# Kernel tuning notes

Hardware: AMD Instinct MI355X
Metric: run time of the kernel (lower is better)

Reference implementation:

```python
import jax, jax.numpy as jnp
import numpy as np

NUM_SAMPLES = 5      # samples per line (line_matcher_cfg)
MIN_DIST_PTS = 8.0   # min pixel spacing between samples
TOP_K = 10           # top-k candidate lines for NW matching
GRID_SIZE = 4        # desc map stride
GAP = 0.1            # NW gap penalty


def sample_line_points(line_seg):
    # line_seg: (N, 2, 2) ij endpoints -> pts (N, S, 2), valid (N, S)
    start, end = line_seg[:, 0], line_seg[:, 1]
    lengths = jnp.linalg.norm(end - start, axis=1)
    nsamp = jnp.clip(jnp.floor(lengths / MIN_DIST_PTS), 2.0, float(NUM_SAMPLES))
    k = jnp.arange(NUM_SAMPLES, dtype=line_seg.dtype)
    interval = (end - start) / (nsamp - 1.0)[:, None]          # (N, 2)
    pts = start[:, None, :] + k[None, :, None] * interval[:, None, :]
    valid = k[None, :] < nsamp[:, None]
    pts = jnp.where(valid[..., None], pts, 0.0)                # torch pads with 0
    return pts, valid


def sample_descriptors(desc, pts):
    # Faithful F.grid_sample(bilinear, zeros padding, align_corners=False) after
    # kornia normalize_pixel_coordinates ((size-1) normalization), then L2-norm.
    # desc: (1, D, H, W); pts: (P, 2) ij coords in full-res image.
    D, H, W = desc.shape[1], desc.shape[2], desc.shape[3]
    img_h, img_w = H * GRID_SIZE, W * GRID_SIZE
    xn = 2.0 * pts[:, 1] / (img_w - 1) - 1.0
    yn = 2.0 * pts[:, 0] / (img_h - 1) - 1.0
    ix = ((xn + 1.0) * W - 1.0) / 2.0   # align_corners=False unnormalize
    iy = ((yn + 1.0) * H - 1.0) / 2.0
    x0f = jnp.floor(ix); y0f = jnp.floor(iy)
    wx = ix - x0f; wy = iy - y0f
    x0 = x0f.astype(jnp.int32); y0 = y0f.astype(jnp.int32)
    img = desc[0]

    def gather(xi, yi):
        inb = ((xi >= 0) & (xi < W) & (yi >= 0) & (yi < H)).astype(img.dtype)
        xc = jnp.clip(xi, 0, W - 1); yc = jnp.clip(yi, 0, H - 1)
        return img[:, yc, xc] * inb[None, :]   # (D, P), zeros outside

    v = (gather(x0, y0) * ((1 - wx) * (1 - wy))[None]
         + gather(x0 + 1, y0) * (wx * (1 - wy))[None]
         + gather(x0, y0 + 1) * ((1 - wx) * wy)[None]
         + gather(x0 + 1, y0 + 1) * (wx * wy)[None])
    return v / jnp.linalg.norm(v, axis=0, keepdims=True)


def needleman_wunsch(scores):
    # scores: (B, n, m); sequential DP via nested lax.scan (rows, then cols)
    B, n, m = scores.shape
    s = jnp.transpose(scores, (1, 0, 2)) - GAP  # (n, B, m)

    def row_step(prev_row, srow):               # prev_row (B, m+1), srow (B, m)
        diag = prev_row[:, :-1].T                # (m, B)
        up = prev_row[:, 1:].T                   # (m, B)

        def col_step(left, xs):
            d, u, sc = xs
            cur = jnp.maximum(jnp.maximum(left, u), d + sc)
            return cur, cur

        _, cols = jax.lax.scan(col_step, jnp.zeros((B,), s.dtype), (diag, up, srow.T))
        new_row = jnp.concatenate([jnp.zeros((B, 1), s.dtype), cols.T], axis=1)
        return new_row, None

    final, _ = jax.lax.scan(row_step, jnp.zeros((B, m + 1), s.dtype), s)
    return final[:, -1]


def filter_and_match_lines(scores):
    # scores: (N, M, n, n)
    ls1 = scores.max(3); v1 = (ls1 != -1.0).astype(scores.dtype)
    ls1 = (ls1 * v1).sum(2) / v1.sum(2)
    ls2 = scores.max(2); v2 = (ls2 != -1.0).astype(scores.dtype)
    ls2 = (ls2 * v2).sum(2) / v2.sum(2)
    line_scores = (ls1 + ls2) / 2.0
    topk_lines = jnp.argsort(line_scores, axis=1)[:, -TOP_K:]          # (N, k)
    top = jnp.take_along_axis(scores, topk_lines[:, :, None, None], axis=1)
    top = jnp.concatenate([top, jnp.flip(top, axis=-1)], axis=1)       # (N, 2k, n, n)
    N, top2k, n, m = top.shape
    nw = needleman_wunsch(top.reshape(N * top2k, n, m)).reshape(N, top2k)
    matches = jnp.argmax(nw, axis=1) % (top2k // 2)
    matches = topk_lines[jnp.arange(N), matches]
    return matches, nw


def match_forward(line_seg1, line_seg2, desc1, desc2):
    N, M = line_seg1.shape[0], line_seg2.shape[0]
    pts1, val1 = sample_line_points(line_seg1)
    pts2, val2 = sample_line_points(line_seg2)
    d1 = sample_descriptors(desc1, pts1.reshape(-1, 2))   # (D, N*S)
    d2 = sample_descriptors(desc2, pts2.reshape(-1, 2))   # (D, M*S)
    scores = d1.T @ d2                                    # (N*S, M*S)
    scores = jnp.where(val1.reshape(-1)[:, None], scores, -1.0)
    scores = jnp.where(val2.reshape(-1)[None, :], scores, -1.0)
    scores = scores.reshape(N, NUM_SAMPLES, M, NUM_SAMPLES).transpose(0, 2, 1, 3)
    matches, nw = filter_and_match_lines(scores)
    # cross check
    matches2, _ = filter_and_match_lines(scores.transpose(1, 0, 3, 2))
    mutual = matches2[matches] == jnp.arange(N)
    matches = jnp.where(mutual, matches, -1)
    return matches, nw


def setup_inputs():
    key = jax.random.key(0)
    k1, k2, k3, k4 = jax.random.split(key, 4)
    N = M = 1200; D = 128; H = W = 128
    img = float(H * GRID_SIZE - 1)
    line_seg1 = jax.random.uniform(k1, (N, 2, 2), jnp.float32) * img
    line_seg2 = jax.random.uniform(k2, (M, 2, 2), jnp.float32) * img
    desc1 = jax.random.normal(k3, (1, D, H, W), jnp.float32)
    desc2 = jax.random.normal(k4, (1, D, H, W), jnp.float32)
    return {"line_seg1": line_seg1, "line_seg2": line_seg2, "desc1": desc1, "desc2": desc2}


def reference(line_seg1, line_seg2, desc1, desc2):
    return match_forward(line_seg1, line_seg2, desc1, desc2)
```

## Files before the change

kernel.cpp:

```cpp
#include <hip/hip_runtime.h>
#include <hip/hip_bf16.h>


#define NLINES 1200
#define NS 5
#define DD 128
#define HH 128
#define WW 128
#define HW (HH*WW)
#define IMGM1 511.0f
#define GAPC 0.1f
#define NPAD 1216
#define PPAD (NPAD*NS)
#define KEXT 384
#define NCH (KEXT/32)
#define NGRP (PPAD/16)

typedef __attribute__((ext_vector_type(8))) short short8;
typedef __attribute__((ext_vector_type(4))) float f32x4;

__global__ void transpose_desc(const float* __restrict__ in1, float* __restrict__ out1,
                               const float* __restrict__ in2, float* __restrict__ out2) {
    const float* in = blockIdx.z ? in2 : in1;
    float* out = blockIdx.z ? out2 : out1;
    __shared__ float t[32][33];
    int s0 = blockIdx.x * 32;
    int d0 = blockIdx.y * 32;
    int c = threadIdx.x;
    int r0 = threadIdx.y;
    #pragma unroll
    for (int rr = 0; rr < 32; rr += 8) {
        int d = d0 + r0 + rr;
        t[r0 + rr][c] = in[d * HW + s0 + c];
    }
    __syncthreads();
    #pragma unroll
    for (int rr = 0; rr < 32; rr += 8) {
        int s = s0 + r0 + rr;
        out[s * DD + d0 + c] = t[c][r0 + rr];
    }
}

__global__ void samplepack_kernel(const float* __restrict__ lseg1, const float* __restrict__ lseg2,
                                  const float* __restrict__ tdesc1, const float* __restrict__ tdesc2,
                                  const float* __restrict__ desc1, const float* __restrict__ desc2,
                                  short* __restrict__ Aext, short* __restrict__ Bext,
                                  float* __restrict__ val1, float* __restrict__ val2,
                                  int use_t) {
    int side = blockIdx.y;
    const float* lseg = side ? lseg2 : lseg1;
    const float* tdesc = side ? tdesc2 : tdesc1;
    const float* desc = side ? desc2 : desc1;
    short* Ef = side ? Bext : Aext;
    float* valout = side ? val2 : val1;
    int arole = side ? 0 : 1;

    __shared__ float ds[16][129];
    int g = blockIdx.x;
    int t = threadIdx.x;
    int lane = t & 63, w = t >> 6;

    #pragma unroll
    for (int s = 0; s < 4; ++s) {
        int r = w * 4 + s;
        int pt = g * 16 + r;
        int line = pt / NS;
        int k = pt - line * NS;

        float sy = 0.f, sx = 0.f, ey = 0.f, ex = 0.f;
        if (line < NLINES) {
            sy = lseg[line * 4 + 0]; sx = lseg[line * 4 + 1];
            ey = lseg[line * 4 + 2]; ex = lseg[line * 4 + 3];
        }
        float dy = ey - sy, dx = ex - sx;
        float len = sqrtf(dy * dy + dx * dx);
        float ns = floorf(len * 0.125f);
        ns = fminf(fmaxf(ns, 2.0f), 5.0f);
        float kf = (float)k;
        float validf = (kf < ns) ? 1.0f : 0.0f;
        float py = sy + kf * (dy / (ns - 1.0f));
        float px = sx + kf * (dx / (ns - 1.0f));
        if (validf == 0.0f) { py = 0.0f; px = 0.0f; }

        float xn = 2.0f * px / IMGM1 - 1.0f;
        float yn = 2.0f * py / IMGM1 - 1.0f;
        float ix = ((xn + 1.0f) * (float)WW - 1.0f) * 0.5f;
        float iy = ((yn + 1.0f) * (float)HH - 1.0f) * 0.5f;
        float x0f = floorf(ix), y0f = floorf(iy);
        float wx = ix - x0f, wy = iy - y0f;
        int x0 = (int)x0f, y0 = (int)y0f;

        float w00 = (1.0f - wx) * (1.0f - wy);
        float w10 = wx * (1.0f - wy);
        float w01 = (1.0f - wx) * wy;
        float w11 = wx * wy;

        float v0 = 0.0f, v1 = 0.0f;
        int xs[4] = { x0, x0 + 1, x0,     x0 + 1 };
        int ys[4] = { y0, y0,     y0 + 1, y0 + 1 };
        float ws4[4] = { w00, w10, w01, w11 };
        #pragma unroll
        for (int c = 0; c < 4; ++c) {
            int xi = xs[c], yi = ys[c];
            float inb = (xi >= 0 && xi < WW && yi >= 0 && yi < HH) ? 1.0f : 0.0f;
            int xc = min(max(xi, 0), WW - 1);
            int yc = min(max(yi, 0), HH - 1);
            if (use_t) {
                int base = (yc * WW + xc) * DD;
                v0 += tdesc[base + lane] * inb * ws4[c];
                v1 += tdesc[base + 64 + lane] * inb * ws4[c];
            } else {
                int base = yc * WW + xc;
                v0 += desc[lane * HW + base] * inb * ws4[c];
                v1 += desc[(lane + 64) * HW + base] * inb * ws4[c];
            }
        }
        float ss = v0 * v0 + v1 * v1;
        #pragma unroll
        for (int o = 32; o > 0; o >>= 1) ss += __shfl_xor(ss, o);
        if (ss == 0.0f) ss = 1.0f;
        float nrm = sqrtf(ss);
        ds[r][lane] = v0 / nrm;
        ds[r][64 + lane] = v1 / nrm;
        if (lane == 0) valout[pt] = (line < NLINES) ? validf : 0.0f;
    }
    __syncthreads();

    #pragma unroll
    for (int it = 0; it < 3; ++it) {
        int idx = it * 256 + t;
        int c = idx >> 6, l = idx & 63;
        int q = l >> 4, r = l & 15;
        short8 outv;
        #pragma unroll
        for (int jj = 0; jj < 8; ++jj) {
            int kext = c * 32 + q * 8 + jj;
            int term = kext >> 7, k = kext & 127;
            float x = ds[r][k];
            __hip_bfloat16 h = __float2bfloat16(x);
            short v = *(short*)&h;
            bool lo_term = arole ? (term == 1) : (term == 2);
            if (lo_term) {
                float hf = __bfloat162float(h);
                __hip_bfloat16 lw = __float2bfloat16(x - hf);
                v = *(short*)&lw;
            }
            outv[jj] = v;
        }
        *(short8*)&Ef[((size_t)(g * NCH + c) * 64 + l) * 8] = outv;
    }
}

__launch_bounds__(256, 2)
__global__ void score_kernel(const short* __restrict__ Af, const short* __restrict__ Bf,
                             const float* __restrict__ val1, const float* __restrict__ val2,
                             float* __restrict__ lsc, float* __restrict__ lscT) {
    __shared__ float dump[80 * 161];

    const int t = threadIdx.x;
    const int lane = t & 63;
    const int w = t >> 6;
    const int wm = w >> 1;
    const int wn = w & 1;
    const int gA0 = blockIdx.x * 10;
    const int gB0 = blockIdx.y * 10;

    const short* pa[5];
    const short* pb[5];
    #pragma unroll
    for (int ti = 0; ti < 5; ++ti) {
        pa[ti] = Af + ((size_t)(gA0 + 5 * wm + ti) * NCH * 64 + lane) * 8;
        pb[ti] = Bf + ((size_t)(gB0 + 5 * wn + ti) * NCH * 64 + lane) * 8;
    }

    f32x4 acc[5][5];
    #pragma unroll
    for (int a = 0; a < 5; ++a)
        #pragma unroll
        for (int b = 0; b < 5; ++b)
            acc[a][b] = (f32x4){0.f, 0.f, 0.f, 0.f};

    short8 ca[5], cb[5], na[5], nb[5];
    #pragma unroll
    for (int ti = 0; ti < 5; ++ti) {
        ca[ti] = *(const short8*)(pa[ti]);
        cb[ti] = *(const short8*)(pb[ti]);
    }
    #pragma unroll
    for (int c = 0; c < NCH; c += 2) {
        #pragma unroll
        for (int ti = 0; ti < 5; ++ti) {
            na[ti] = *(const short8*)(pa[ti] + (c + 1) * 512);
            nb[ti] = *(const short8*)(pb[ti] + (c + 1) * 512);
        }
        #pragma unroll
        for (int ti = 0; ti < 5; ++ti)
            #pragma unroll
            for (int tj = 0; tj < 5; ++tj)
                acc[ti][tj] = __builtin_amdgcn_mfma_f32_16x16x32_bf16(
                    ca[ti], cb[tj], acc[ti][tj], 0, 0, 0);
        if (c + 2 < NCH) {
            #pragma unroll
            for (int ti = 0; ti < 5; ++ti) {
                ca[ti] = *(const short8*)(pa[ti] + (c + 2) * 512);
                cb[ti] = *(const short8*)(pb[ti] + (c + 2) * 512);
            }
        }
        #pragma unroll
        for (int ti = 0; ti < 5; ++ti)
            #pragma unroll
            for (int tj = 0; tj < 5; ++tj)
                acc[ti][tj] = __builtin_amdgcn_mfma_f32_16x16x32_bf16(
                    na[ti], nb[tj], acc[ti][tj], 0, 0, 0);
    }

    const int i0l = blockIdx.x * 32;
    const int j0l = blockIdx.y * 32;
    #pragma unroll
    for (int p = 0; p < 2; ++p) {
        __syncthreads();
        if (wm == p) {
            #pragma unroll
            for (int ti = 0; ti < 5; ++ti) {
                #pragma unroll
                for (int reg = 0; reg < 4; ++reg) {
                    int rloc = 16 * ti + (lane >> 4) * 4 + reg;
                    #pragma unroll
                    for (int tj = 0; tj < 5; ++tj) {
                        int col = 80 * wn + 16 * tj + (lane & 15);
                        dump[rloc * 161 + col] = acc[ti][tj][reg];
                    }
                }
            }
        }
        __syncthreads();
        #pragma unroll
        for (int e = 0; e < 2; ++e) {
            int q = t * 2 + e;
            int li = q >> 5, lj = q & 31;
            int i = i0l + 16 * p + li;
            int j = j0l + lj;
            if (i < NLINES && j < NLINES) {
                float S[5][5];
                #pragma unroll
                for (int a = 0; a < 5; ++a) {
                    float va = val1[i * NS + a];
                    #pragma unroll
                    for (int b = 0; b < 5; ++b) {
                        float vb = val2[j * NS + b];
                        float sc = dump[(li * 5 + a) * 161 + (lj * 5 + b)];
                        S[a][b] = (va != 0.0f && vb != 0.0f) ? sc : -1.0f;
                    }
                }
                float sum1 = 0.0f, cnt1 = 0.0f;
                #pragma unroll
                for (int a = 0; a < 5; ++a) {
                    float r = S[a][0];
                    #pragma unroll
                    for (int b = 1; b < 5; ++b) r = fmaxf(r, S[a][b]);
                    float v = (r != -1.0f) ? 1.0f : 0.0f;
                    sum1 += r * v; cnt1 += v;
                }
                float sum2 = 0.0f, cnt2 = 0.0f;
                #pragma unroll
                for (int b = 0; b < 5; ++b) {
                    float r = S[0][b];
                    #pragma unroll
                    for (int a = 1; a < 5; ++a) r = fmaxf(r, S[a][b]);
                    float v = (r != -1.0f) ? 1.0f : 0.0f;
                    sum2 += r * v; cnt2 += v;
                }
                lsc[i * NLINES + j] = (sum1 / cnt1 + sum2 / cnt2) * 0.5f;
            }
        }
        #pragma unroll
        for (int e = 0; e < 2; ++e) {
            int q = t * 2 + e;
            int lj = q >> 4, li = q & 15;
            int i = i0l + 16 * p + li;
            int j = j0l + lj;
            if (i < NLINES && j < NLINES) {
                float S[5][5];
                #pragma unroll
                for (int a = 0; a < 5; ++a) {
                    float va = val1[i * NS + a];
                    #pragma unroll
                    for (int b = 0; b < 5; ++b) {
                        float vb = val2[j * NS + b];
                        float sc = dump[(li * 5 + a) * 161 + (lj * 5 + b)];
                        S[a][b] = (va != 0.0f && vb != 0.0f) ? sc : -1.0f;
                    }
                }
                float sum1 = 0.0f, cnt1 = 0.0f;
                #pragma unroll
                for (int a = 0; a < 5; ++a) {
                    float r = S[a][0];
                    #pragma unroll
                    for (int b = 1; b < 5; ++b) r = fmaxf(r, S[a][b]);
                    float v = (r != -1.0f) ? 1.0f : 0.0f;
                    sum1 += r * v; cnt1 += v;
                }
                float sum2 = 0.0f, cnt2 = 0.0f;
                #pragma unroll
                for (int b = 0; b < 5; ++b) {
                    float r = S[0][b];
                    #pragma unroll
                    for (int a = 1; a < 5; ++a) r = fmaxf(r, S[a][b]);
                    float v = (r != -1.0f) ? 1.0f : 0.0f;
                    sum2 += r * v; cnt2 += v;
                }
                lscT[j * NLINES + i] = (sum1 / cnt1 + sum2 / cnt2) * 0.5f;
            }
        }
    }
}

__global__ void topk_kernel(const float* __restrict__ lsc, const float* __restrict__ lscT,
                            int* __restrict__ topk1, int* __restrict__ topk2) {
    __shared__ float wv[4];
    __shared__ int wi[4];
    int rb = blockIdx.x;
    const float* ls = (rb < NLINES) ? (lsc + rb * NLINES) : (lscT + (rb - NLINES) * NLINES);
    int* topk = (rb < NLINES) ? (topk1 + rb * 10) : (topk2 + (rb - NLINES) * 10);
    int t = threadIdx.x;
    int lane = t & 63, w = t >> 6;
    float val[5];
    #pragma unroll
    for (int s = 0; s < 5; ++s) {
        int j = t + 256 * s;
        val[s] = (j < NLINES) ? ls[j] : -1e30f;
    }
    float bv = -1e30f; int bi = -1;
    #pragma unroll
    for (int s = 0; s < 5; ++s) {
        int j = t + 256 * s;
        if (val[s] >= bv) { bv = val[s]; bi = j; }
    }
    for (int sel = 0; sel < 10; ++sel) {
        float rv = bv; int ri = bi;
        #pragma unroll
        for (int o = 32; o > 0; o >>= 1) {
            float ov = __shfl_xor(rv, o);
            int oi = __shfl_xor(ri, o);
            if (ov > rv || (ov == rv && oi > ri)) { rv = ov; ri = oi; }
        }
        if (lane == 0) { wv[w] = rv; wi[w] = ri; }
        __syncthreads();
        float fv = wv[0]; int fi = wi[0];
        #pragma unroll
        for (int qq = 1; qq < 4; ++qq)
            if (wv[qq] > fv || (wv[qq] == fv && wi[qq] > fi)) { fv = wv[qq]; fi = wi[qq]; }
        if (t == 0) topk[9 - sel] = fi;
        if ((fi & 255) == t) {
            val[fi >> 8] = -1e30f;
            bv = -1e30f; bi = -1;
            #pragma unroll
            for (int s = 0; s < 5; ++s) {
                int j = t + 256 * s;
                if (val[s] >= bv) { bv = val[s]; bi = j; }
            }
        }
        __syncthreads();
    }
}

__device__ __forceinline__ float nw5(const float* M) {
    float F[6] = {0, 0, 0, 0, 0, 0};
    #pragma unroll
    for (int x = 0; x < 5; ++x) {
        float diag = F[0];
        float left = 0.0f;
        #pragma unroll
        for (int y = 1; y <= 5; ++y) {
            float up = F[y];
            float cur = fmaxf(fmaxf(left, up), diag + (M[x * 5 + y - 1] - GAPC));
            F[y] = cur; left = cur; diag = up;
        }
    }
    return F[5];
}

__global__ void nw_kernel(const short* __restrict__ Af, const short* __restrict__ Bf,
                          const float* __restrict__ val1, const float* __restrict__ val2,
                          const int* __restrict__ topk1, const int* __restrict__ topk2,
                          float* __restrict__ nwout, float* __restrict__ nw2buf) {
    __shared__ float sbuf[10][25];
    __shared__ int jl[10];
    int rb = blockIdx.x;
    int dir = (rb >= NLINES) ? 1 : 0;
    int row = rb - dir * NLINES;
    int lane = threadIdx.x;
    int q = lane >> 4, rr = lane & 15;

    if (lane < 10) jl[lane] = (dir ? topk2 : topk1)[row * 10 + lane];
    __syncthreads();

    const short* shEf = dir ? Bf : Af;
    const short* cdEf = dir ? Af : Bf;

    int ptS = row * 5 + min(rr, 4);
    const short* shp = shEf + ((size_t)(ptS >> 4) * NCH * 64 + q * 16 + (ptS & 15)) * 8;
    short8 sh[NCH];
    #pragma unroll
    for (int c = 0; c < NCH; ++c) sh[c] = *(const short8*)(shp + c * 512);

    #pragma unroll
    for (int pp = 0; pp < 5; ++pp) {
        int c1 = jl[2 * pp], c2 = jl[2 * pp + 1];
        int ptC = (rr < 8) ? (c1 * 5 + min(rr, 4)) : (c2 * 5 + min(rr - 8, 4));
        const short* cp = cdEf + ((size_t)(ptC >> 4) * NCH * 64 + q * 16 + (ptC & 15)) * 8;
        f32x4 acc = (f32x4){0.f, 0.f, 0.f, 0.f};
        #pragma unroll
        for (int c = 0; c < NCH; ++c) {
            short8 cb = *(const short8*)(cp + c * 512);
            acc = dir ? __builtin_amdgcn_mfma_f32_16x16x32_bf16(cb, sh[c], acc, 0, 0, 0)
                      : __builtin_amdgcn_mfma_f32_16x16x32_bf16(sh[c], cb, acc, 0, 0, 0);
        }
        #pragma unroll
        for (int reg = 0; reg < 4; ++reg) {
            int m = q * 4 + reg, n = rr;
            if (!dir) {
                if (m < 5 && n < 5) sbuf[2 * pp][m * 5 + n] = acc[reg];
                if (m < 5 && n >= 8 && n < 13) sbuf[2 * pp + 1][m * 5 + (n - 8)] = acc[reg];
            } else {
                if (m < 5 && n < 5) sbuf[2 * pp][m * 5 + n] = acc[reg];
                if (m >= 8 && m < 13 && n < 5) sbuf[2 * pp + 1][(m - 8) * 5 + n] = acc[reg];
            }
        }
    }
    __syncthreads();

    if (lane < 20) {
        int r = lane >> 1, rev = lane & 1;
        int i = dir ? jl[r] : row;
        int j = dir ? row : jl[r];
        float S[25];
        #pragma unroll
        for (int a = 0; a < 5; ++a) {
            float va = val1[i * NS + a];
            #pragma unroll
            for (int b = 0; b < 5; ++b) {
                float vb = val2[j * NS + b];
                S[a * 5 + b] = (va != 0.0f && vb != 0.0f) ? sbuf[r][a * 5 + b] : -1.0f;
            }
        }
        float M[25];
        #pragma unroll
        for (int x = 0; x < 5; ++x)
            #pragma unroll
            for (int y = 0; y < 5; ++y) {
                if (!dir) M[x * 5 + y] = rev ? S[x * 5 + (4 - y)] : S[x * 5 + y];
                else      M[x * 5 + y] = rev ? S[(4 - y) * 5 + x] : S[y * 5 + x];
            }
        float nwv = nw5(M);
        float* o = dir ? nw2buf : nwout;
        o[row * 20 + rev * 10 + r] = nwv;
    }
}

__global__ void argmax_final_kernel(const float* __restrict__ nw1, const float* __restrict__ nw2,
                                    const int* __restrict__ topk1, const int* __restrict__ topk2,
                                    float* __restrict__ out) {
    __shared__ int mpre[NLINES];
    __shared__ int m2[NLINES];
    int t = threadIdx.x;
    for (int qq = t; qq < 2 * NLINES; qq += 1024) {
        int dir = qq / NLINES, row = qq - dir * NLINES;
        const float* nw = (dir ? nw2 : nw1) + row * 20;
        float best = nw[0]; int bi = 0;
        #pragma unroll
        for (int q = 1; q < 20; ++q) {
            float v = nw[q];
            if (v > best) { best = v; bi = q; }
        }
        int m = (dir ? topk2 : topk1)[row * 10 + (bi % 10)];
        if (dir) m2[row] = m; else mpre[row] = m;
    }
    __syncthreads();
    for (int i = t; i < NLINES; i += 1024) {
        int m = mpre[i];
        out[i] = (m2[m] == i) ? (float)m : -1.0f;
    }
}

extern "C" void kernel_launch(void* const* d_in, const int* in_sizes, int n_in,
                              void* d_out, int out_size, void* d_ws, size_t ws_size,
                              hipStream_t stream) {
    const float* lseg1 = (const float*)d_in[0];
    const float* lseg2 = (const float*)d_in[1];
    const float* desc1 = (const float*)d_in[2];
    const float* desc2 = (const float*)d_in[3];
    float* out = (float*)d_out;

    float* wsf = (float*)d_ws;
    size_t off = 0;
    float* val1 = wsf + off;   off += PPAD;
    float* val2 = wsf + off;   off += PPAD;
    float* lsc = wsf + off;    off += (size_t)NLINES * NLINES;
    float* lscT = wsf + off;   off += (size_t)NLINES * NLINES;
    int* topk1 = (int*)(wsf + off); off += NLINES * 10;
    int* topk2 = (int*)(wsf + off); off += NLINES * 10;
    float* nw2buf = wsf + off; off += NLINES * 20;
    short* Aext = (short*)(wsf + off); off += (size_t)PPAD * KEXT / 2;
    short* Bext = (short*)(wsf + off); off += (size_t)PPAD * KEXT / 2;
    float* tdesc1 = wsf + off; off += (size_t)HW * DD;
    float* tdesc2 = wsf + off; off += (size_t)HW * DD;
    size_t need_full = off * sizeof(float);
    int use_t = (ws_size >= need_full) ? 1 : 0;

    if (use_t) {
        transpose_desc<<<dim3(HW / 32, DD / 32, 2), dim3(32, 8), 0, stream>>>(
            desc1, tdesc1, desc2, tdesc2);
    }
    samplepack_kernel<<<dim3(NGRP, 2), 256, 0, stream>>>(
        lseg1, lseg2, tdesc1, tdesc2, desc1, desc2, Aext, Bext, val1, val2, use_t);

    score_kernel<<<dim3(NPAD / 32, NPAD / 32), 256, 0, stream>>>(Aext, Bext, val1, val2,
                                                                 lsc, lscT);

    topk_kernel<<<2 * NLINES, 256, 0, stream>>>(lsc, lscT, topk1, topk2);

    nw_kernel<<<2 * NLINES, 64, 0, stream>>>(Aext, Bext, val1, val2, topk1, topk2,
                                             out + NLINES, nw2buf);

    argmax_final_kernel<<<1, 1024, 0, stream>>>(out + NLINES, nw2buf, topk1, topk2, out);
}
```

Before: 197.6 us.

## Vectorize descriptor transpose, dedupe score epilogue, split NW MFMA across five waves

The descriptor transpose now moves float4 values through a wider 32x128 shared tile, which cuts the number of load and store instructions. The score epilogue computes each line-pair score once, stages it in a shared buffer and writes the transposed copy from there, instead of repeating the full 5x5 reduction for lscT. The NW kernel launches 320 threads so each of five waves handles one candidate pair with its own MFMA chain, rather than one wave looping over all five. The cost is more shared memory and an extra barrier in the score kernel, plus redundant reloads of the shared-line descriptor in every NW wave.

```diff
diff --git a/kernel.cpp b/kernel.cpp
--- a/kernel.cpp
+++ b/kernel.cpp
@@ -23,21 +23,24 @@
                                const float* __restrict__ in2, float* __restrict__ out2) {
     const float* in = blockIdx.z ? in2 : in1;
     float* out = blockIdx.z ? out2 : out1;
-    __shared__ float t[32][33];
-    int s0 = blockIdx.x * 32;
+    __shared__ float t[32][132];
+    int s0 = blockIdx.x * 128;
     int d0 = blockIdx.y * 32;
-    int c = threadIdx.x;
-    int r0 = threadIdx.y;
-    #pragma unroll
-    for (int rr = 0; rr < 32; rr += 8) {
-        int d = d0 + r0 + rr;
-        t[r0 + rr][c] = in[d * HW + s0 + c];
+    int tid = threadIdx.x;
+    #pragma unroll
+    for (int pass = 0; pass < 4; ++pass) {
+        int idx = pass * 256 + tid;
+        int dr = idx >> 5, si = idx & 31;
+        float4 v = *(const float4*)&in[(size_t)(d0 + dr) * HW + s0 + 4 * si];
+        *(float4*)&t[dr][4 * si] = v;
     }
     __syncthreads();
     #pragma unroll
-    for (int rr = 0; rr < 32; rr += 8) {
-        int s = s0 + r0 + rr;
-        out[s * DD + d0 + c] = t[c][r0 + rr];
+    for (int pass = 0; pass < 4; ++pass) {
+        int idx = pass * 256 + tid;
+        int sr = idx >> 3, di = idx & 7;
+        float4 v = { t[4 * di][sr], t[4 * di + 1][sr], t[4 * di + 2][sr], t[4 * di + 3][sr] };
+        *(float4*)&out[(size_t)(s0 + sr) * DD + d0 + 4 * di] = v;
     }
 }
 
@@ -156,6 +159,7 @@
                              const float* __restrict__ val1, const float* __restrict__ val2,
                              float* __restrict__ lsc, float* __restrict__ lscT) {
     __shared__ float dump[80 * 161];
+    __shared__ float red[16][33];
 
     const int t = threadIdx.x;
     const int lane = t & 63;
@@ -240,77 +244,47 @@
             int li = q >> 5, lj = q & 31;
             int i = i0l + 16 * p + li;
             int j = j0l + lj;
-            if (i < NLINES && j < NLINES) {
-                float S[5][5];
-                #pragma unroll
-                for (int a = 0; a < 5; ++a) {
-                    float va = val1[i * NS + a];
-                    #pragma unroll
-                    for (int b = 0; b < 5; ++b) {
-                        float vb = val2[j * NS + b];
-                        float sc = dump[(li * 5 + a) * 161 + (lj * 5 + b)];
-                        S[a][b] = (va != 0.0f && vb != 0.0f) ? sc : -1.0f;
-                    }
-                }
-                float sum1 = 0.0f, cnt1 = 0.0f;
-                #pragma unroll
-                for (int a = 0; a < 5; ++a) {
-                    float r = S[a][0];
-                    #pragma unroll
-                    for (int b = 1; b < 5; ++b) r = fmaxf(r, S[a][b]);
-                    float v = (r != -1.0f) ? 1.0f : 0.0f;
-                    sum1 += r * v; cnt1 += v;
-                }
-                float sum2 = 0.0f, cnt2 = 0.0f;
+            float S[5][5];
+            #pragma unroll
+            for (int a = 0; a < 5; ++a) {
+                float va = val1[i * NS + a];
                 #pragma unroll
                 for (int b = 0; b < 5; ++b) {
-                    float r = S[0][b];
-                    #pragma unroll
-                    for (int a = 1; a < 5; ++a) r = fmaxf(r, S[a][b]);
-                    float v = (r != -1.0f) ? 1.0f : 0.0f;
-                    sum2 += r * v; cnt2 += v;
+                    float vb = val2[j * NS + b];
+                    float sc = dump[(li * 5 + a) * 161 + (lj * 5 + b)];
+                    S[a][b] = (va != 0.0f && vb != 0.0f) ? sc : -1.0f;
                 }
-                lsc[i * NLINES + j] = (sum1 / cnt1 + sum2 / cnt2) * 0.5f;
-            }
-        }
+            }
+            float sum1 = 0.0f, cnt1 = 0.0f;
+            #pragma unroll
+            for (int a = 0; a < 5; ++a) {
+                float r = S[a][0];
+                #pragma unroll
+                for (int b = 1; b < 5; ++b) r = fmaxf(r, S[a][b]);
+                float v = (r != -1.0f) ? 1.0f : 0.0f;
+                sum1 += r * v; cnt1 += v;
+            }
+            float sum2 = 0.0f, cnt2 = 0.0f;
+            #pragma unroll
+            for (int b = 0; b < 5; ++b) {
+                float r = S[0][b];
+                #pragma unroll
+                for (int a = 1; a < 5; ++a) r = fmaxf(r, S[a][b]);
+                float v = (r != -1.0f) ? 1.0f : 0.0f;
+                sum2 += r * v; cnt2 += v;
+            }
+            float res = (sum1 / cnt1 + sum2 / cnt2) * 0.5f;
+            red[li][lj] = res;
+            if (i < NLINES && j < NLINES) lsc[i * NLINES + j] = res;
+        }
+        __syncthreads();
         #pragma unroll
         for (int e = 0; e < 2; ++e) {
-            int q = t * 2 + e;
-            int lj = q >> 4, li = q & 15;
+            int q = t + 256 * e;
+            int li = q & 15, lj = q >> 4;
             int i = i0l + 16 * p + li;
             int j = j0l + lj;
-            if (i < NLINES && j < NLINES) {
-                float S[5][5];
-                #pragma unroll
-                for (int a = 0; a < 5; ++a) {
-                    float va = val1[i * NS + a];
-                    #pragma unroll
-                    for (int b = 0; b < 5; ++b) {
-                        float vb = val2[j * NS + b];
-                        float sc = dump[(li * 5 + a) * 161 + (lj * 5 + b)];
-                        S[a][b] = (va != 0.0f && vb != 0.0f) ? sc : -1.0f;
-                    }
-                }
-                float sum1 = 0.0f, cnt1 = 0.0f;
-                #pragma unroll
-                for (int a = 0; a < 5; ++a) {
-                    float r = S[a][0];
-                    #pragma unroll
-                    for (int b = 1; b < 5; ++b) r = fmaxf(r, S[a][b]);
-                    float v = (r != -1.0f) ? 1.0f : 0.0f;
-                    sum1 += r * v; cnt1 += v;
-                }
-                float sum2 = 0.0f, cnt2 = 0.0f;
-                #pragma unroll
-                for (int b = 0; b < 5; ++b) {
-                    float r = S[0][b];
-                    #pragma unroll
-                    for (int a = 1; a < 5; ++a) r = fmaxf(r, S[a][b]);
-                    float v = (r != -1.0f) ? 1.0f : 0.0f;
-                    sum2 += r * v; cnt2 += v;
-                }
-                lscT[j * NLINES + i] = (sum1 / cnt1 + sum2 / cnt2) * 0.5f;
-            }
+            if (i < NLINES && j < NLINES) lscT[j * NLINES + i] = red[li][lj];
         }
     }
 }
@@ -389,10 +363,12 @@
     int rb = blockIdx.x;
     int dir = (rb >= NLINES) ? 1 : 0;
     int row = rb - dir * NLINES;
-    int lane = threadIdx.x;
+    int t = threadIdx.x;
+    int w = t >> 6;
+    int lane = t & 63;
     int q = lane >> 4, rr = lane & 15;
 
-    if (lane < 10) jl[lane] = (dir ? topk2 : topk1)[row * 10 + lane];
+    if (t < 10) jl[t] = (dir ? topk2 : topk1)[row * 10 + t];
     __syncthreads();
 
     const short* shEf = dir ? Bf : Af;
@@ -400,38 +376,34 @@
 
     int ptS = row * 5 + min(rr, 4);
     const short* shp = shEf + ((size_t)(ptS >> 4) * NCH * 64 + q * 16 + (ptS & 15)) * 8;
-    short8 sh[NCH];
-    #pragma unroll
-    for (int c = 0; c < NCH; ++c) sh[c] = *(const short8*)(shp + c * 512);
-
-    #pragma unroll
-    for (int pp = 0; pp < 5; ++pp) {
-        int c1 = jl[2 * pp], c2 = jl[2 * pp + 1];
-        int ptC = (rr < 8) ? (c1 * 5 + min(rr, 4)) : (c2 * 5 + min(rr - 8, 4));
-        const short* cp = cdEf + ((size_t)(ptC >> 4) * NCH * 64 + q * 16 + (ptC & 15)) * 8;
-        f32x4 acc = (f32x4){0.f, 0.f, 0.f, 0.f};
-        #pragma unroll
-        for (int c = 0; c < NCH; ++c) {
-            short8 cb = *(const short8*)(cp + c * 512);
-            acc = dir ? __builtin_amdgcn_mfma_f32_16x16x32_bf16(cb, sh[c], acc, 0, 0, 0)
-                      : __builtin_amdgcn_mfma_f32_16x16x32_bf16(sh[c], cb, acc, 0, 0, 0);
-        }
-        #pragma unroll
-        for (int reg = 0; reg < 4; ++reg) {
-            int m = q * 4 + reg, n = rr;
-            if (!dir) {
-                if (m < 5 && n < 5) sbuf[2 * pp][m * 5 + n] = acc[reg];
-                if (m < 5 && n >= 8 && n < 13) sbuf[2 * pp + 1][m * 5 + (n - 8)] = acc[reg];
-            } else {
-                if (m < 5 && n < 5) sbuf[2 * pp][m * 5 + n] = acc[reg];
-                if (m >= 8 && m < 13 && n < 5) sbuf[2 * pp + 1][(m - 8) * 5 + n] = acc[reg];
-            }
+
+    int c1 = jl[2 * w], c2 = jl[2 * w + 1];
+    int ptC = (rr < 8) ? (c1 * 5 + min(rr, 4)) : (c2 * 5 + min(rr - 8, 4));
+    const short* cp = cdEf + ((size_t)(ptC >> 4) * NCH * 64 + q * 16 + (ptC & 15)) * 8;
+
+    f32x4 acc = (f32x4){0.f, 0.f, 0.f, 0.f};
+    #pragma unroll
+    for (int c = 0; c < NCH; ++c) {
+        short8 sh = *(const short8*)(shp + c * 512);
+        short8 cb = *(const short8*)(cp + c * 512);
+        acc = dir ? __builtin_amdgcn_mfma_f32_16x16x32_bf16(cb, sh, acc, 0, 0, 0)
+                  : __builtin_amdgcn_mfma_f32_16x16x32_bf16(sh, cb, acc, 0, 0, 0);
+    }
+    #pragma unroll
+    for (int reg = 0; reg < 4; ++reg) {
+        int m = q * 4 + reg, n = rr;
+        if (!dir) {
+            if (m < 5 && n < 5) sbuf[2 * w][m * 5 + n] = acc[reg];
+            if (m < 5 && n >= 8 && n < 13) sbuf[2 * w + 1][m * 5 + (n - 8)] = acc[reg];
+        } else {
+            if (m < 5 && n < 5) sbuf[2 * w][m * 5 + n] = acc[reg];
+            if (m >= 8 && m < 13 && n < 5) sbuf[2 * w + 1][(m - 8) * 5 + n] = acc[reg];
         }
     }
     __syncthreads();
 
-    if (lane < 20) {
-        int r = lane >> 1, rev = lane & 1;
+    if (t < 20) {
+        int r = t >> 1, rev = t & 1;
         int i = dir ? jl[r] : row;
         int j = dir ? row : jl[r];
         float S[25];
@@ -509,7 +481,7 @@
     int use_t = (ws_size >= need_full) ? 1 : 0;
 
     if (use_t) {
-        transpose_desc<<<dim3(HW / 32, DD / 32, 2), dim3(32, 8), 0, stream>>>(
+        transpose_desc<<<dim3(HW / 128, DD / 32, 2), 256, 0, stream>>>(
             desc1, tdesc1, desc2, tdesc2);
     }
     samplepack_kernel<<<dim3(NGRP, 2), 256, 0, stream>>>(
@@ -520,8 +492,8 @@
 
     topk_kernel<<<2 * NLINES, 256, 0, stream>>>(lsc, lscT, topk1, topk2);
 
-    nw_kernel<<<2 * NLINES, 64, 0, stream>>>(Aext, Bext, val1, val2, topk1, topk2,
-                                             out + NLINES, nw2buf);
+    nw_kernel<<<2 * NLINES, 320, 0, stream>>>(Aext, Bext, val1, val2, topk1, topk2,
+                                              out + NLINES, nw2buf);
 
     argmax_final_kernel<<<1, 1024, 0, stream>>>(out + NLINES, nw2buf, topk1, topk2, out);
 }
```

New measurement: 183.0 us. 7.4% less time.
